# Kernel tuning notes

Hardware: AMD Instinct MI355X
Metric: run time of the kernel (lower is better)

Reference implementation:

```python
import jax, jax.numpy as jnp
import numpy as np

EPS = 1e-4  # LayerNorm epsilon from module


def layer_norm(x):
    # torch: (x - mean) / (std + eps), std unbiased (ddof=1), no affine
    mean = jnp.mean(x, axis=-1, keepdims=True)
    std = jnp.sqrt(jnp.var(x, axis=-1, ddof=1, keepdims=True))
    return (x - mean) / (std + EPS)


def setup_inputs() -> dict:
    key = jax.random.key(0)
    ks = jax.random.split(key, 9)
    B, S, D, H, QK = 2, 2048, 1024, 16, 64
    E = D // H  # per-head value/output dim
    scale = 0.02
    x = jax.random.normal(ks[0], (B, S, D), dtype=jnp.float32)
    # stacked per-head projection weights, Linear as x @ W + b
    Wq = jax.random.normal(ks[1], (H, D, QK), dtype=jnp.float32) * scale
    bq = jax.random.normal(ks[2], (H, QK), dtype=jnp.float32) * scale
    Wk = jax.random.normal(ks[3], (H, D, QK), dtype=jnp.float32) * scale
    bk = jax.random.normal(ks[4], (H, QK), dtype=jnp.float32) * scale
    Wv = jax.random.normal(ks[5], (H, D, E), dtype=jnp.float32) * scale
    bv = jax.random.normal(ks[6], (H, E), dtype=jnp.float32) * scale
    Wff = jax.random.normal(ks[7], (D, D), dtype=jnp.float32) * scale
    bff = jax.random.normal(ks[8], (D,), dtype=jnp.float32) * scale
    return {"x": x, "Wq": Wq, "bq": bq, "Wk": Wk, "bk": bk,
            "Wv": Wv, "bv": bv, "Wff": Wff, "bff": bff}


def reference(x, Wq, bq, Wk, bk, Wv, bv, Wff, bff):
    B, S, D = x.shape
    # all heads at once (vectorized over the Python per-head loop)
    Q = jnp.einsum('bsd,hdq->bhsq', x, Wq) + bq[None, :, None, :]
    K = jnp.einsum('bsd,hdq->bhsq', x, Wk) + bk[None, :, None, :]
    V = jnp.einsum('bsd,hde->bhse', x, Wv) + bv[None, :, None, :]
    scores = jnp.einsum('bhsq,bhtq->bhst', Q, K)  # [B,H,S,S]
    # masked_fill on tril(..., diagonal=-1): strictly-lower entries -> -inf
    mask = jnp.tril(jnp.ones((S, S), dtype=bool), k=-1)
    scores = jnp.where(mask[None, None], -jnp.inf, scores)
    # non-standard softmax axis: dim=-2 (over rows s, not keys t)
    attn = jax.nn.softmax(scores, axis=-2)
    heads = jnp.einsum('bhst,bhte->bhse', attn, V)  # [B,H,S,E]
    H, E = heads.shape[1], heads.shape[3]
    combined = heads.transpose(0, 2, 1, 3).reshape(B, S, H * E)  # concat heads
    x = layer_norm(x + combined)
    x = x + (x @ Wff + bff)
    return layer_norm(x)
```

## Files before the change

### kernel.cpp

```cpp
#include <hip/hip_runtime.h>
#include <hip/hip_bf16.h>
#include <math.h>

typedef unsigned short u16;
typedef unsigned int u32;
typedef __attribute__((ext_vector_type(8))) short short8;
typedef __attribute__((ext_vector_type(4))) short short4v;
typedef __attribute__((ext_vector_type(4))) float f32x4;

constexpr int B  = 2;
constexpr int S  = 2048;
constexpr int D  = 1024;
constexpr int H  = 16;
constexpr int DK = 64;
constexpr int BS = B * S;
constexpr float LOG2E = 1.4426950408889634f;

__device__ __forceinline__ u16 f2b(float f) {
    __hip_bfloat16 h = __float2bfloat16(f);
    return *reinterpret_cast<u16*>(&h);
}
__device__ __forceinline__ float b2f(short s) {
    unsigned int u = ((unsigned int)(u16)s) << 16;
    return __builtin_bit_cast(float, u);
}
__device__ __forceinline__ float fexp2(float x) { return __builtin_exp2f(x); }

#define MFMA16(a, b, c) __builtin_amdgcn_mfma_f32_16x16x32_bf16((a), (b), (c), 0, 0, 0)

__device__ __forceinline__ void gload16(const u16* g, u16* l) {
    __builtin_amdgcn_global_load_lds(
        (const __attribute__((address_space(1))) u32*)g,
        (__attribute__((address_space(3))) u32*)l, 16, 0, 0);
}

__global__ __launch_bounds__(256) void convert_x(const float* __restrict__ src,
                                                 u16* __restrict__ dst)
{
    size_t i = ((size_t)blockIdx.x * 256 + threadIdx.x) * 8;
    f32x4 a = *reinterpret_cast<const f32x4*>(src + i);
    f32x4 b = *reinterpret_cast<const f32x4*>(src + i + 4);
    short8 o;
    o[0] = (short)f2b(a[0]); o[1] = (short)f2b(a[1]);
    o[2] = (short)f2b(a[2]); o[3] = (short)f2b(a[3]);
    o[4] = (short)f2b(b[0]); o[5] = (short)f2b(b[1]);
    o[6] = (short)f2b(b[2]); o[7] = (short)f2b(b[3]);
    *reinterpret_cast<short8*>(dst + i) = o;
}

__global__ __launch_bounds__(256) void tconv(const float* __restrict__ src,
                                             u16* __restrict__ dst, int R, int C)
{
    const int bb = blockIdx.z;
    src += (size_t)bb * R * C;
    dst += (size_t)bb * R * C;
    const int c0 = blockIdx.x * 64, r0 = blockIdx.y * 64;
    __shared__ float Ts[64][65];
    const int tid = threadIdx.x;
    #pragma unroll
    for (int i = 0; i < 4; ++i) {
        int idx = i * 1024 + tid * 4;
        int r = idx >> 6, c = idx & 63;
        f32x4 v = *reinterpret_cast<const f32x4*>(&src[(size_t)(r0 + r) * C + c0 + c]);
        Ts[r][c] = v[0]; Ts[r][c + 1] = v[1]; Ts[r][c + 2] = v[2]; Ts[r][c + 3] = v[3];
    }
    __syncthreads();
    #pragma unroll
    for (int i = 0; i < 4; ++i) {
        int cc = i * 16 + (tid >> 4);
        int rr = (tid & 15) * 4;
        short4v pk;
        pk[0] = (short)f2b(Ts[rr][cc]);     pk[1] = (short)f2b(Ts[rr + 1][cc]);
        pk[2] = (short)f2b(Ts[rr + 2][cc]); pk[3] = (short)f2b(Ts[rr + 3][cc]);
        *reinterpret_cast<short4v*>(&dst[(size_t)(c0 + cc) * R + r0 + rr]) = pk;
    }
}

__global__ __launch_bounds__(256) void tconv3(
    const float* __restrict__ wq, const float* __restrict__ wk,
    const float* __restrict__ wv, u16* __restrict__ dst)
{
    const int z = blockIdx.z;
    const int selw = z >> 4, bb = z & 15;
    const float* src = selw == 0 ? wq : selw == 1 ? wk : wv;
    src += (size_t)bb * D * DK;
    u16* d = dst + (size_t)selw * H * DK * D + (size_t)bb * D * DK;
    const int r0 = blockIdx.y * 64;
    __shared__ float Ts[64][65];
    const int tid = threadIdx.x;
    #pragma unroll
    for (int i = 0; i < 4; ++i) {
        int idx = i * 1024 + tid * 4;
        int r = idx >> 6, c = idx & 63;
        f32x4 v = *reinterpret_cast<const f32x4*>(&src[(size_t)(r0 + r) * DK + c]);
        Ts[r][c] = v[0]; Ts[r][c + 1] = v[1]; Ts[r][c + 2] = v[2]; Ts[r][c + 3] = v[3];
    }
    __syncthreads();
    #pragma unroll
    for (int i = 0; i < 4; ++i) {
        int cc = i * 16 + (tid >> 4);
        int rr = (tid & 15) * 4;
        short4v pk;
        pk[0] = (short)f2b(Ts[rr][cc]);     pk[1] = (short)f2b(Ts[rr + 1][cc]);
        pk[2] = (short)f2b(Ts[rr + 2][cc]); pk[3] = (short)f2b(Ts[rr + 3][cc]);
        *reinterpret_cast<short4v*>(&d[(size_t)cc * D + r0 + rr]) = pk;
    }
}

__global__ __launch_bounds__(256) void qkv_gemm(
    const u16* __restrict__ xb, const u16* __restrict__ WT,
    const float* __restrict__ bq, const float* __restrict__ bk, const float* __restrict__ bv,
    u16* __restrict__ Qw, u16* __restrict__ Kw, u16* __restrict__ Vtw)
{
    const int id   = blockIdx.x;
    const int xcd  = id & 7;
    const int j    = id >> 3;
    const int nblk = xcd * 3 + j % 3;
    const int mblk = j / 3;
    const int m0 = mblk * 128, n0 = nblk * 128;
    const int sel = n0 >> 10;
    const float* bias = sel == 0 ? bq : sel == 1 ? bk : bv;
    const float qscale = (sel == 0) ? LOG2E : 1.0f;

    __shared__ u16 SM[2][2][128][64];

    const int tid = threadIdx.x;
    const int w = tid >> 6, ln = tid & 15, hi = (tid & 63) >> 4;
    const int wm = w >> 1, wn = w & 1;
    const int l  = tid & 63;
    const int lr = l >> 3;
    const int lc8 = ((l & 7) ^ lr) * 8;

    char* sA0 = (char*)&SM[0][0][0][0];
    char* sB0 = (char*)&SM[0][1][0][0];
    char* sA1 = (char*)&SM[1][0][0][0];
    char* sB1 = (char*)&SM[1][1][0][0];
    auto swz = [](int r, int cb) { return r * 128 + (cb ^ ((r & 7) << 4)); };

    f32x4 acc[4][4];
    #pragma unroll
    for (int m = 0; m < 4; ++m)
        #pragma unroll
        for (int n = 0; n < 4; ++n) acc[m][n] = f32x4{0.f, 0.f, 0.f, 0.f};

    auto stage = [&](char* sa, char* sb, int k0) {
        #pragma unroll
        for (int c = 0; c < 4; ++c) {
            int rbase = w * 32 + c * 8;
            int row = rbase + lr;
            gload16(&xb[(size_t)(m0 + row) * D + k0 + lc8], (u16*)(sa + rbase * 128));
            gload16(&WT[(size_t)(n0 + row) * D + k0 + lc8], (u16*)(sb + rbase * 128));
        }
    };

    stage(sA0, sB0, 0);
    __syncthreads();

    for (int it = 0; it < 16; ++it) {
        char* ac = (it & 1) ? sA1 : sA0;
        char* bc = (it & 1) ? sB1 : sB0;
        if (it + 1 < 16)
            stage((it & 1) ? sA0 : sA1, (it & 1) ? sB0 : sB1, (it + 1) * 64);
        #pragma unroll
        for (int ks = 0; ks < 2; ++ks) {
            short8 af[4], bf[4];
            #pragma unroll
            for (int m = 0; m < 4; ++m)
                af[m] = *reinterpret_cast<const short8*>(
                    ac + swz(wm * 64 + m * 16 + ln, ks * 64 + hi * 16));
            #pragma unroll
            for (int n = 0; n < 4; ++n)
                bf[n] = *reinterpret_cast<const short8*>(
                    bc + swz(wn * 64 + n * 16 + ln, ks * 64 + hi * 16));
            #pragma unroll
            for (int m = 0; m < 4; ++m)
                #pragma unroll
                for (int n = 0; n < 4; ++n)
                    acc[m][n] = MFMA16(af[m], bf[n], acc[m][n]);
        }
        __syncthreads();
    }

    float bias4[4];
    #pragma unroll
    for (int n = 0; n < 4; ++n)
        bias4[n] = bias[(n0 & 1023) + wn * 64 + n * 16 + ln];

    char* eb = sA0;
    const int bidx  = m0 >> 11;
    const int sbase = m0 & 2047;
    const int h0    = (n0 & 1023) >> 6;

    if (sel < 2) {
        #pragma unroll
        for (int m = 0; m < 4; ++m)
            #pragma unroll
            for (int n = 0; n < 4; ++n)
                #pragma unroll
                for (int r = 0; r < 4; ++r) {
                    int row = wm * 64 + m * 16 + hi * 4 + r;
                    int col = wn * 64 + n * 16 + ln;
                    *reinterpret_cast<u16*>(eb + row * 256 + ((col * 2) ^ ((row & 7) << 4))) =
                        f2b((acc[m][n][r] + bias4[n]) * qscale);
                }
        __syncthreads();
        u16* dst0 = sel == 0 ? Qw : Kw;
        #pragma unroll
        for (int c = 0; c < 8; ++c) {
            int idx = c * 256 + tid;
            int row = idx >> 4, g = idx & 15;
            short8 v = *reinterpret_cast<const short8*>(
                eb + row * 256 + ((g * 16) ^ ((row & 7) << 4)));
            int h = h0 + (g >> 3), j0 = (g & 7) * 8;
            *reinterpret_cast<short8*>(
                &dst0[((size_t)(bidx * H + h) * S + sbase + row) * DK + j0]) = v;
        }
    } else {
        #pragma unroll
        for (int m = 0; m < 4; ++m)
            #pragma unroll
            for (int n = 0; n < 4; ++n)
                #pragma unroll
                for (int r = 0; r < 4; ++r) {
                    int row = wm * 64 + m * 16 + hi * 4 + r;
                    int col = wn * 64 + n * 16 + ln;
                    *reinterpret_cast<u16*>(eb + col * 256 + ((row * 2) ^ ((col & 7) << 4))) =
                        f2b(acc[m][n][r] + bias4[n]);
                }
        __syncthreads();
        #pragma unroll
        for (int c = 0; c < 8; ++c) {
            int idx = c * 256 + tid;
            int e = idx >> 4, g = idx & 15;
            short8 v = *reinterpret_cast<const short8*>(
                eb + e * 256 + ((g * 16) ^ ((e & 7) << 4)));
            int h = h0 + (e >> 6), ein = e & 63;
            *reinterpret_cast<short8*>(
                &Vtw[((size_t)(bidx * H + h) * DK + ein) * S + sbase + g * 8]) = v;
        }
    }
}

__global__ __launch_bounds__(256) void col_stats(
    const u16* __restrict__ Qw, const u16* __restrict__ Kw,
    u16* __restrict__ Vtw)
{
    const int id = blockIdx.x;
    const int bh = (id & 7) * 4 + ((id >> 3) & 3);
    const int t0 = (31 - (id >> 5)) * 64;
    const u16* Qh = Qw + (size_t)bh * S * DK;
    const u16* Kh = Kw + (size_t)bh * S * DK;
    u16* Vh = Vtw + (size_t)bh * DK * S;

    __shared__ u16 Qs[2][64][64];
    __shared__ float zbuf[64];

    const int tid = threadIdx.x;
    const int w = tid >> 6, ln = tid & 15, hi = (tid & 63) >> 4;
    const int e0 = tid >> 3, sc = tid & 7;
    const int l = tid & 63, lr = l >> 3;
    const int lc8 = ((l & 7) ^ lr) * 8;

    char* qb0 = (char*)&Qs[0][0][0];
    char* qb1 = (char*)&Qs[1][0][0];
    auto swz = [](int row, int colb) { return (row * 128 + colb) ^ ((row & 7) << 4); };

    auto stageQ = [&](char* buf, int s) {
        #pragma unroll
        for (int c = 0; c < 2; ++c) {
            int rbase = w * 16 + c * 8;
            gload16(&Qh[(size_t)(s + rbase + lr) * DK + lc8], (u16*)(buf + rbase * 128));
        }
    };

    short8 ak[2];
    #pragma unroll
    for (int ks = 0; ks < 2; ++ks)
        ak[ks] = *reinterpret_cast<const short8*>(
            &Kh[(size_t)(t0 + w * 16 + ln) * DK + ks * 32 + hi * 8]);

    float zs[4] = {0.f, 0.f, 0.f, 0.f};

    auto qk = [&](char* qb, f32x4 (&c)[4]) {
        #pragma unroll
        for (int n = 0; n < 4; ++n) c[n] = f32x4{0.f, 0.f, 0.f, 0.f};
        __builtin_amdgcn_s_setprio(1);
        #pragma unroll
        for (int ks = 0; ks < 2; ++ks)
            #pragma unroll
            for (int n = 0; n < 4; ++n) {
                short8 bqf = *reinterpret_cast<const short8*>(
                    qb + swz(n * 16 + ln, ks * 64 + hi * 16));
                c[n] = MFMA16(ak[ks], bqf, c[n]);
            }
        __builtin_amdgcn_s_setprio(0);
    };

    stageQ(qb0, 0);
    __syncthreads();

    int cur = 0;
    for (int s0b = 0; s0b < t0; s0b += 64) {
        stageQ(cur ? qb0 : qb1, s0b + 64);
        f32x4 c[4];
        qk(cur ? qb1 : qb0, c);
        #pragma unroll
        for (int n = 0; n < 4; ++n)
            #pragma unroll
            for (int r = 0; r < 4; ++r)
                zs[r] += fexp2(c[n][r]);
        __syncthreads();
        cur ^= 1;
    }
    {
        f32x4 c[4];
        qk(cur ? qb1 : qb0, c);
        #pragma unroll
        for (int n = 0; n < 4; ++n)
            #pragma unroll
            for (int r = 0; r < 4; ++r) {
                float v = (n * 16 + ln > w * 16 + hi * 4 + r) ? 0.f : fexp2(c[n][r]);
                zs[r] += v;
            }
    }

    #pragma unroll
    for (int r = 0; r < 4; ++r) {
        #pragma unroll
        for (int msk = 1; msk < 16; msk <<= 1)
            zs[r] += __shfl_xor(zs[r], msk, 64);
    }
    if (ln == 0) {
        #pragma unroll
        for (int r = 0; r < 4; ++r)
            zbuf[w * 16 + hi * 4 + r] = 1.f / zs[r];
    }
    __syncthreads();

    float iz[8];
    #pragma unroll
    for (int j = 0; j < 8; ++j) iz[j] = zbuf[sc * 8 + j];
    #pragma unroll
    for (int pass = 0; pass < 2; ++pass) {
        int e = e0 + 32 * pass;
        u16* vp = &Vh[(size_t)e * S + t0 + sc * 8];
        short8 v = *reinterpret_cast<short8*>(vp);
        short8 o;
        #pragma unroll
        for (int j = 0; j < 8; ++j) o[j] = (short)f2b(b2f(v[j]) * iz[j]);
        *reinterpret_cast<short8*>(vp) = o;
    }
}

__global__ __launch_bounds__(256) void attn_pv(
    const u16* __restrict__ Qw, const u16* __restrict__ Kw, const u16* __restrict__ Vtw,
    float* __restrict__ combined)
{
    const int id = blockIdx.x;
    const int bh = (id & 7) * 4 + ((id >> 3) & 3);
    const int s0 = (id >> 5) * 64;
    const int bidx = bh >> 4, h = bh & 15;
    const u16* Qh = Qw + (size_t)bh * S * DK;
    const u16* Kh = Kw + (size_t)bh * S * DK;
    const u16* Vh = Vtw + (size_t)bh * DK * S;

    __shared__ u16 Vs[2][64][64];
    __shared__ u16 Ps[64][72];

    const int tid = threadIdx.x;
    const int w = tid >> 6, ln = tid & 15, hi = (tid & 63) >> 4;
    const int l = tid & 63, lr = l >> 3;
    const int lc8 = ((l & 7) ^ lr) * 8;

    char* vb0 = (char*)&Vs[0][0][0];
    char* vb1 = (char*)&Vs[1][0][0];
    auto swz = [](int row, int colb) { return (row * 128 + colb) ^ ((row & 7) << 4); };

    auto stageV = [&](char* buf, int t) {
        #pragma unroll
        for (int c = 0; c < 2; ++c) {
            int rbase = w * 16 + c * 8;
            gload16(&Vh[(size_t)(rbase + lr) * S + t + lc8], (u16*)(buf + rbase * 128));
        }
    };

    short8 bq[4][2];
    #pragma unroll
    for (int n = 0; n < 4; ++n)
        #pragma unroll
        for (int ks = 0; ks < 2; ++ks)
            bq[n][ks] = *reinterpret_cast<const short8*>(
                &Qh[(size_t)(s0 + n * 16 + ln) * DK + ks * 32 + hi * 8]);

    f32x4 acc[4];
    #pragma unroll
    for (int n = 0; n < 4; ++n) acc[n] = f32x4{0.f, 0.f, 0.f, 0.f};

    short8 akA[2], akB[2];
    auto loadK = [&](short8 (&ak)[2], int t1) {
        #pragma unroll
        for (int ks = 0; ks < 2; ++ks)
            ak[ks] = *reinterpret_cast<const short8*>(
                &Kh[(size_t)(t1 + w * 16 + ln) * DK + ks * 32 + hi * 8]);
    };

    auto proc = [&](short8 (&ak)[2], char* vb, bool diag) {
        f32x4 st[4];
        #pragma unroll
        for (int n = 0; n < 4; ++n) st[n] = f32x4{0.f, 0.f, 0.f, 0.f};
        __builtin_amdgcn_s_setprio(1);
        #pragma unroll
        for (int ks = 0; ks < 2; ++ks)
            #pragma unroll
            for (int n = 0; n < 4; ++n)
                st[n] = MFMA16(ak[ks], bq[n][ks], st[n]);
        __builtin_amdgcn_s_setprio(0);

        #pragma unroll
        for (int n = 0; n < 4; ++n) {
            short4v pk;
            #pragma unroll
            for (int r = 0; r < 4; ++r) {
                float pv = fexp2(st[n][r]);
                if (diag && (n * 16 + ln) > (w * 16 + hi * 4 + r)) pv = 0.f;
                pk[r] = (short)f2b(pv);
            }
            *reinterpret_cast<short4v*>(&Ps[n * 16 + ln][w * 16 + hi * 4]) = pk;
        }
        __syncthreads();

        short8 pa[2];
        #pragma unroll
        for (int ks = 0; ks < 2; ++ks)
            pa[ks] = *reinterpret_cast<const short8*>(&Ps[w * 16 + ln][ks * 32 + hi * 8]);
        __builtin_amdgcn_s_setprio(1);
        #pragma unroll
        for (int ks = 0; ks < 2; ++ks)
            #pragma unroll
            for (int n = 0; n < 4; ++n) {
                short8 vv = *reinterpret_cast<const short8*>(
                    vb + swz(n * 16 + ln, ks * 64 + hi * 16));
                acc[n] = MFMA16(pa[ks], vv, acc[n]);
            }
        __builtin_amdgcn_s_setprio(0);
        __syncthreads();
    };

    stageV(vb0, s0);
    loadK(akA, s0);
    __syncthreads();

    int t1 = s0;
    if (t1 + 64 < S) { stageV(vb1, t1 + 64); loadK(akB, t1 + 64); }
    proc(akA, vb0, true);
    t1 += 64;

    while (t1 < S) {
        if (t1 + 64 < S) { stageV(vb0, t1 + 64); loadK(akA, t1 + 64); }
        proc(akB, vb1, false);
        t1 += 64;
        if (t1 >= S) break;
        if (t1 + 64 < S) { stageV(vb1, t1 + 64); loadK(akB, t1 + 64); }
        proc(akA, vb0, false);
        t1 += 64;
    }

    #pragma unroll
    for (int n = 0; n < 4; ++n)
        #pragma unroll
        for (int r = 0; r < 4; ++r) {
            int s = s0 + w * 16 + hi * 4 + r;
            combined[((size_t)bidx * S + s) * D + h * DK + n * 16 + ln] = acc[n][r];
        }
}

__global__ __launch_bounds__(256) void add_ln(
    const float* __restrict__ a, const float* __restrict__ bsrc,
    float* __restrict__ out, u16* __restrict__ outb)
{
    const int row = blockIdx.x;
    const int tid = threadIdx.x;
    const size_t base = (size_t)row * D;

    float v[4];
    float sum = 0.f;
    #pragma unroll
    for (int i = 0; i < 4; ++i) {
        int c = tid + i * 256;
        float t = a[base + c];
        if (bsrc) t += bsrc[base + c];
        v[i] = t;
        sum += t;
    }

    __shared__ float red[8];
    #pragma unroll
    for (int o = 32; o > 0; o >>= 1) sum += __shfl_down(sum, o, 64);
    const int lane = tid & 63, w = tid >> 6;
    if (lane == 0) red[w] = sum;
    __syncthreads();
    const float mean = (red[0] + red[1] + red[2] + red[3]) * (1.f / D);

    float s2 = 0.f;
    #pragma unroll
    for (int i = 0; i < 4; ++i) { float d2 = v[i] - mean; s2 += d2 * d2; }
    #pragma unroll
    for (int o = 32; o > 0; o >>= 1) s2 += __shfl_down(s2, o, 64);
    if (lane == 0) red[4 + w] = s2;
    __syncthreads();
    const float var = (red[4] + red[5] + red[6] + red[7]) * (1.f / (D - 1));
    const float scale = 1.f / (sqrtf(var) + 1e-4f);

    #pragma unroll
    for (int i = 0; i < 4; ++i) {
        int c = tid + i * 256;
        float o = (v[i] - mean) * scale;
        out[base + c] = o;
        if (outb) outb[base + c] = f2b(o);
    }
}

__global__ __launch_bounds__(256) void ffn(
    const float* __restrict__ x1, const u16* __restrict__ x1b,
    const u16* __restrict__ WffT, const float* __restrict__ bff,
    float* __restrict__ x2)
{
    const int id = blockIdx.x;
    const int m0 = ((id & 7) * 4 + ((id >> 3) & 3)) * 128;
    const int n0 = (id >> 5) * 128;

    __shared__ u16 SM[2][2][128][64];

    const int tid = threadIdx.x;
    const int w = tid >> 6, ln = tid & 15, hi = (tid & 63) >> 4;
    const int wm = w >> 1, wn = w & 1;
    const int l  = tid & 63;
    const int lr = l >> 3;
    const int lc8 = ((l & 7) ^ lr) * 8;

    char* sA0 = (char*)&SM[0][0][0][0];
    char* sB0 = (char*)&SM[0][1][0][0];
    char* sA1 = (char*)&SM[1][0][0][0];
    char* sB1 = (char*)&SM[1][1][0][0];
    auto swz = [](int r, int cb) { return r * 128 + (cb ^ ((r & 7) << 4)); };

    f32x4 acc[4][4];
    #pragma unroll
    for (int m = 0; m < 4; ++m)
        #pragma unroll
        for (int n = 0; n < 4; ++n) acc[m][n] = f32x4{0.f, 0.f, 0.f, 0.f};

    auto stage = [&](char* sa, char* sb, int k0) {
        #pragma unroll
        for (int c = 0; c < 4; ++c) {
            int rbase = w * 32 + c * 8;
            int row = rbase + lr;
            gload16(&x1b[(size_t)(m0 + row) * D + k0 + lc8], (u16*)(sa + rbase * 128));
            gload16(&WffT[(size_t)(n0 + row) * D + k0 + lc8], (u16*)(sb + rbase * 128));
        }
    };

    stage(sA0, sB0, 0);
    __syncthreads();

    for (int it = 0; it < 16; ++it) {
        char* ac = (it & 1) ? sA1 : sA0;
        char* bc = (it & 1) ? sB1 : sB0;
        if (it + 1 < 16)
            stage((it & 1) ? sA0 : sA1, (it & 1) ? sB0 : sB1, (it + 1) * 64);
        #pragma unroll
        for (int ks = 0; ks < 2; ++ks) {
            short8 af[4], bf[4];
            #pragma unroll
            for (int m = 0; m < 4; ++m)
                af[m] = *reinterpret_cast<const short8*>(
                    ac + swz(wm * 64 + m * 16 + ln, ks * 64 + hi * 16));
            #pragma unroll
            for (int n = 0; n < 4; ++n)
                bf[n] = *reinterpret_cast<const short8*>(
                    bc + swz(wn * 64 + n * 16 + ln, ks * 64 + hi * 16));
            #pragma unroll
            for (int m = 0; m < 4; ++m)
                #pragma unroll
                for (int n = 0; n < 4; ++n)
                    acc[m][n] = MFMA16(af[m], bf[n], acc[m][n]);
        }
        __syncthreads();
    }

    float bf4[4];
    #pragma unroll
    for (int n = 0; n < 4; ++n) bf4[n] = bff[n0 + wn * 64 + n * 16 + ln];

    #pragma unroll
    for (int m = 0; m < 4; ++m)
        #pragma unroll
        for (int n = 0; n < 4; ++n)
            #pragma unroll
            for (int r = 0; r < 4; ++r) {
                int row = m0 + wm * 64 + m * 16 + hi * 4 + r;
                int col = n0 + wn * 64 + n * 16 + ln;
                size_t idx = (size_t)row * D + col;
                x2[idx] = x1[idx] + acc[m][n][r] + bf4[n];
            }
}

extern "C" void kernel_launch(void* const* d_in, const int* in_sizes, int n_in,
                              void* d_out, int out_size, void* d_ws, size_t ws_size,
                              hipStream_t stream)
{
    const float* x   = (const float*)d_in[0];
    const float* Wq  = (const float*)d_in[1];
    const float* bq  = (const float*)d_in[2];
    const float* Wk  = (const float*)d_in[3];
    const float* bk  = (const float*)d_in[4];
    const float* Wv  = (const float*)d_in[5];
    const float* bv  = (const float*)d_in[6];
    const float* Wff = (const float*)d_in[7];
    const float* bff = (const float*)d_in[8];
    float* out = (float*)d_out;

    const size_t NX = (size_t)BS * D;
    char* p = (char*)d_ws;
    auto alloc = [&](size_t bytes) { char* r = p; p += bytes; return r; };

    u16* xb    = (u16*)alloc(NX * 2);
    u16* WT    = (u16*)alloc((size_t)3 * H * DK * D * 2);
    u16* WffT  = (u16*)alloc((size_t)D * D * 2);
    u16* Qw    = (u16*)alloc(NX * 2);
    u16* Kw    = (u16*)alloc(NX * 2);
    u16* Vtw   = (u16*)alloc(NX * 2);
    float* combined = (float*)alloc(NX * 4);
    float* x1       = (float*)alloc(NX * 4);
    u16*   x1b = xb;
    float* x2  = (float*)Qw;

    convert_x<<<dim3(NX / 2048), 256, 0, stream>>>(x, xb);
    tconv3<<<dim3(1, 16, 48), 256, 0, stream>>>(Wq, Wk, Wv, WT);
    tconv<<<dim3(16, 16, 1), 256, 0, stream>>>(Wff, WffT, D, D);

    qkv_gemm<<<dim3(768), 256, 0, stream>>>(
        xb, WT, bq, bk, bv, Qw, Kw, Vtw);

    col_stats<<<dim3(1024), 256, 0, stream>>>(Qw, Kw, Vtw);

    attn_pv<<<dim3(1024), 256, 0, stream>>>(Qw, Kw, Vtw, combined);

    add_ln<<<BS, 256, 0, stream>>>(x, combined, x1, x1b);

    ffn<<<dim3(256), 256, 0, stream>>>(x1, x1b, WffT, bff, x2);

    add_ln<<<BS, 256, 0, stream>>>(x2, nullptr, out, nullptr);
}
```

Before: 153.3 us.

## Register-prefetch Q/V tiles into LDS, store combined in bf16, vectorize add_ln

In col_stats and attn_pv, the asynchronous global-to-LDS gload16 staging is replaced by register prefetch. Each thread issues its global loads for the next tile early and writes them to swizzled LDS after the MFMA work on the current tile. The attention output `combined` is now written as bf16 instead of fp32, which halves that intermediate's traffic but adds rounding before the residual LayerNorm. add_ln now uses contiguous 4-wide vector loads and stores per thread instead of strided scalar accesses.

```diff
diff --git a/kernel.cpp b/kernel.cpp
--- a/kernel.cpp
+++ b/kernel.cpp
@@ -258,20 +258,10 @@
     const int tid = threadIdx.x;
     const int w = tid >> 6, ln = tid & 15, hi = (tid & 63) >> 4;
     const int e0 = tid >> 3, sc = tid & 7;
-    const int l = tid & 63, lr = l >> 3;
-    const int lc8 = ((l & 7) ^ lr) * 8;
 
     char* qb0 = (char*)&Qs[0][0][0];
     char* qb1 = (char*)&Qs[1][0][0];
     auto swz = [](int row, int colb) { return (row * 128 + colb) ^ ((row & 7) << 4); };
-
-    auto stageQ = [&](char* buf, int s) {
-        #pragma unroll
-        for (int c = 0; c < 2; ++c) {
-            int rbase = w * 16 + c * 8;
-            gload16(&Qh[(size_t)(s + rbase + lr) * DK + lc8], (u16*)(buf + rbase * 128));
-        }
-    };
 
     short8 ak[2];
     #pragma unroll
@@ -296,12 +286,18 @@
         __builtin_amdgcn_s_setprio(0);
     };
 
-    stageQ(qb0, 0);
+    {
+        short8 a = *reinterpret_cast<const short8*>(&Qh[(size_t)e0 * DK + sc * 8]);
+        short8 b = *reinterpret_cast<const short8*>(&Qh[(size_t)(e0 + 32) * DK + sc * 8]);
+        *reinterpret_cast<short8*>(qb0 + swz(e0, sc * 16)) = a;
+        *reinterpret_cast<short8*>(qb0 + swz(e0 + 32, sc * 16)) = b;
+    }
     __syncthreads();
 
     int cur = 0;
     for (int s0b = 0; s0b < t0; s0b += 64) {
-        stageQ(cur ? qb0 : qb1, s0b + 64);
+        short8 nq0 = *reinterpret_cast<const short8*>(&Qh[(size_t)(s0b + 64 + e0) * DK + sc * 8]);
+        short8 nq1 = *reinterpret_cast<const short8*>(&Qh[(size_t)(s0b + 96 + e0) * DK + sc * 8]);
         f32x4 c[4];
         qk(cur ? qb1 : qb0, c);
         #pragma unroll
@@ -309,6 +305,9 @@
             #pragma unroll
             for (int r = 0; r < 4; ++r)
                 zs[r] += fexp2(c[n][r]);
+        char* qn = cur ? qb0 : qb1;
+        *reinterpret_cast<short8*>(qn + swz(e0, sc * 16)) = nq0;
+        *reinterpret_cast<short8*>(qn + swz(e0 + 32, sc * 16)) = nq1;
         __syncthreads();
         cur ^= 1;
     }
@@ -318,10 +317,8 @@
         #pragma unroll
         for (int n = 0; n < 4; ++n)
             #pragma unroll
-            for (int r = 0; r < 4; ++r) {
-                float v = (n * 16 + ln > w * 16 + hi * 4 + r) ? 0.f : fexp2(c[n][r]);
-                zs[r] += v;
-            }
+            for (int r = 0; r < 4; ++r)
+                zs[r] += (n * 16 + ln > w * 16 + hi * 4 + r) ? 0.f : fexp2(c[n][r]);
     }
 
     #pragma unroll
@@ -354,7 +351,7 @@
 
 __global__ __launch_bounds__(256) void attn_pv(
     const u16* __restrict__ Qw, const u16* __restrict__ Kw, const u16* __restrict__ Vtw,
-    float* __restrict__ combined)
+    u16* __restrict__ combined)
 {
     const int id = blockIdx.x;
     const int bh = (id & 7) * 4 + ((id >> 3) & 3);
@@ -369,20 +366,11 @@
 
     const int tid = threadIdx.x;
     const int w = tid >> 6, ln = tid & 15, hi = (tid & 63) >> 4;
-    const int l = tid & 63, lr = l >> 3;
-    const int lc8 = ((l & 7) ^ lr) * 8;
+    const int e0 = tid >> 3, sc = tid & 7;
 
     char* vb0 = (char*)&Vs[0][0][0];
     char* vb1 = (char*)&Vs[1][0][0];
     auto swz = [](int row, int colb) { return (row * 128 + colb) ^ ((row & 7) << 4); };
-
-    auto stageV = [&](char* buf, int t) {
-        #pragma unroll
-        for (int c = 0; c < 2; ++c) {
-            int rbase = w * 16 + c * 8;
-            gload16(&Vh[(size_t)(rbase + lr) * S + t + lc8], (u16*)(buf + rbase * 128));
-        }
-    };
 
     short8 bq[4][2];
     #pragma unroll
@@ -404,7 +392,14 @@
                 &Kh[(size_t)(t1 + w * 16 + ln) * DK + ks * 32 + hi * 8]);
     };
 
-    auto proc = [&](short8 (&ak)[2], char* vb, bool diag) {
+    auto proc = [&](short8 (&ak)[2], char* vbc, char* vbn, bool diag, int t1) {
+        const bool nxt = (t1 + 64 < S);
+        short8 nv0, nv1;
+        if (nxt) {
+            nv0 = *reinterpret_cast<const short8*>(&Vh[(size_t)e0 * S + t1 + 64 + sc * 8]);
+            nv1 = *reinterpret_cast<const short8*>(&Vh[(size_t)(e0 + 32) * S + t1 + 64 + sc * 8]);
+        }
+
         f32x4 st[4];
         #pragma unroll
         for (int n = 0; n < 4; ++n) st[n] = f32x4{0.f, 0.f, 0.f, 0.f};
@@ -439,29 +434,39 @@
             #pragma unroll
             for (int n = 0; n < 4; ++n) {
                 short8 vv = *reinterpret_cast<const short8*>(
-                    vb + swz(n * 16 + ln, ks * 64 + hi * 16));
+                    vbc + swz(n * 16 + ln, ks * 64 + hi * 16));
                 acc[n] = MFMA16(pa[ks], vv, acc[n]);
             }
         __builtin_amdgcn_s_setprio(0);
+
+        if (nxt) {
+            *reinterpret_cast<short8*>(vbn + swz(e0, sc * 16)) = nv0;
+            *reinterpret_cast<short8*>(vbn + swz(e0 + 32, sc * 16)) = nv1;
+        }
         __syncthreads();
     };
 
-    stageV(vb0, s0);
+    {
+        short8 a = *reinterpret_cast<const short8*>(&Vh[(size_t)e0 * S + s0 + sc * 8]);
+        short8 b = *reinterpret_cast<const short8*>(&Vh[(size_t)(e0 + 32) * S + s0 + sc * 8]);
+        *reinterpret_cast<short8*>(vb0 + swz(e0, sc * 16)) = a;
+        *reinterpret_cast<short8*>(vb0 + swz(e0 + 32, sc * 16)) = b;
+    }
     loadK(akA, s0);
     __syncthreads();
 
     int t1 = s0;
-    if (t1 + 64 < S) { stageV(vb1, t1 + 64); loadK(akB, t1 + 64); }
-    proc(akA, vb0, true);
+    if (t1 + 64 < S) loadK(akB, t1 + 64);
+    proc(akA, vb0, vb1, true, t1);
     t1 += 64;
 
     while (t1 < S) {
-        if (t1 + 64 < S) { stageV(vb0, t1 + 64); loadK(akA, t1 + 64); }
-        proc(akB, vb1, false);
+        if (t1 + 64 < S) loadK(akA, t1 + 64);
+        proc(akB, vb1, vb0, false, t1);
         t1 += 64;
         if (t1 >= S) break;
-        if (t1 + 64 < S) { stageV(vb1, t1 + 64); loadK(akB, t1 + 64); }
-        proc(akA, vb0, false);
+        if (t1 + 64 < S) loadK(akB, t1 + 64);
+        proc(akA, vb0, vb1, false, t1);
         t1 += 64;
     }
 
@@ -470,27 +475,28 @@
         #pragma unroll
         for (int r = 0; r < 4; ++r) {
             int s = s0 + w * 16 + hi * 4 + r;
-            combined[((size_t)bidx * S + s) * D + h * DK + n * 16 + ln] = acc[n][r];
+            combined[((size_t)bidx * S + s) * D + h * DK + n * 16 + ln] = f2b(acc[n][r]);
         }
 }
 
 __global__ __launch_bounds__(256) void add_ln(
-    const float* __restrict__ a, const float* __restrict__ bsrc,
+    const float* __restrict__ a, const u16* __restrict__ bsrc,
     float* __restrict__ out, u16* __restrict__ outb)
 {
     const int row = blockIdx.x;
     const int tid = threadIdx.x;
-    const size_t base = (size_t)row * D;
-
+    const size_t base = (size_t)row * D + tid * 4;
+
+    f32x4 xa = *reinterpret_cast<const f32x4*>(a + base);
     float v[4];
     float sum = 0.f;
-    #pragma unroll
-    for (int i = 0; i < 4; ++i) {
-        int c = tid + i * 256;
-        float t = a[base + c];
-        if (bsrc) t += bsrc[base + c];
-        v[i] = t;
-        sum += t;
+    if (bsrc) {
+        short4v cb = *reinterpret_cast<const short4v*>(bsrc + base);
+        #pragma unroll
+        for (int i = 0; i < 4; ++i) { v[i] = xa[i] + b2f(cb[i]); sum += v[i]; }
+    } else {
+        #pragma unroll
+        for (int i = 0; i < 4; ++i) { v[i] = xa[i]; sum += v[i]; }
     }
 
     __shared__ float red[8];
@@ -511,13 +517,15 @@
     const float var = (red[4] + red[5] + red[6] + red[7]) * (1.f / (D - 1));
     const float scale = 1.f / (sqrtf(var) + 1e-4f);
 
+    f32x4 o4;
+    short4v ob;
     #pragma unroll
     for (int i = 0; i < 4; ++i) {
-        int c = tid + i * 256;
-        float o = (v[i] - mean) * scale;
-        out[base + c] = o;
-        if (outb) outb[base + c] = f2b(o);
-    }
+        o4[i] = (v[i] - mean) * scale;
+        ob[i] = (short)f2b(o4[i]);
+    }
+    *reinterpret_cast<f32x4*>(out + base) = o4;
+    if (outb) *reinterpret_cast<short4v*>(outb + base) = ob;
 }
 
 __global__ __launch_bounds__(256) void ffn(
@@ -630,8 +638,8 @@
     u16* Qw    = (u16*)alloc(NX * 2);
     u16* Kw    = (u16*)alloc(NX * 2);
     u16* Vtw   = (u16*)alloc(NX * 2);
-    float* combined = (float*)alloc(NX * 4);
-    float* x1       = (float*)alloc(NX * 4);
+    u16* combined = (u16*)alloc(NX * 2);
+    float* x1     = (float*)alloc(NX * 4);
     u16*   x1b = xb;
     float* x2  = (float*)Qw;
 
```

Result: no change. 153.9 us (+0.4%).
